# Performance work log

Measured on AMD Instinct MI355X. Metric: run time of the kernel, lower is better.

## Reference

```python
import jax, jax.numpy as jnp
import numpy as np

W = H = 64
CONFIGS = [(1, 3), (2, 3), (3, 3)]  # (dilation, kernel_size)
OUT_PER_CFG = 32
IN_CH = 32


def build_mask():
    # One (W+1, H+1) mask per config, broadcast over (out, in) channels.
    masks = []
    for d, k in CONFIGS:
        m = np.zeros((W + 1, H + 1), dtype=np.float32)
        k1 = (k - 1) * (d - 1) + k  # effective dilated kernel extent
        s1 = (W - k1) // 2 + 1
        e1 = (W + k1) // 2 + 1
        s2 = (H - k1) // 2 + 1
        e2 = (H + k1) // 2 + 1
        m[s1:e1:d, s2:e2:d] = 1.0
        masks.append(np.broadcast_to(m, (OUT_PER_CFG, 1, W + 1, H + 1)))
    return jnp.asarray(np.concatenate(masks, axis=0))  # (96, 1, 65, 65)


def setup_inputs() -> dict:
    key = jax.random.key(0)
    k1, k2 = jax.random.split(key)
    x = jax.random.normal(k1, (16, IN_CH, W, H), dtype=jnp.float32)
    # small init so tanh does not saturate
    weight = jax.random.normal(k2, (OUT_PER_CFG * len(CONFIGS), IN_CH, W + 1, H + 1), dtype=jnp.float32) * 0.01
    mask = build_mask()
    gamma = jnp.ones((OUT_PER_CFG * len(CONFIGS),), dtype=jnp.float32)
    beta = jnp.zeros((OUT_PER_CFG * len(CONFIGS),), dtype=jnp.float32)
    return {"x": x, "weight": weight, "mask": mask, "gamma": gamma, "beta": beta}


def reference(x, weight, mask, gamma, beta):
    # circular pad: last dim by H//2 each side, dim -2 by W//2 each side
    xp = jnp.pad(x, ((0, 0), (0, 0), (W // 2, W // 2), (H // 2, H // 2)), mode="wrap")
    y = jax.lax.conv_general_dilated(
        xp, weight * mask,
        window_strides=(1, 1), padding="VALID",
        dimension_numbers=("NCHW", "OIHW", "NCHW"),
    )  # (B, 96, 64, 64)
    # BatchNorm2d in training mode: batch statistics over (N, H, W), eps=1e-5
    mean = jnp.mean(y, axis=(0, 2, 3))
    var = jnp.var(y, axis=(0, 2, 3))
    yn = (y - mean[None, :, None, None]) * jax.lax.rsqrt(var + 1e-5)[None, :, None, None]
    yn = yn * gamma[None, :, None, None] + beta[None, :, None, None]
    return jnp.tanh(yn)
```

## Files before the change

### kernel.cpp

```cpp
#include <hip/hip_runtime.h>
#include <math.h>

#define BATCH 16
#define CIN 32
#define COUT 96
#define WH 64
#define IMG (WH*WH)
#define NPIX (BATCH*IMG)
#define YELEMS (BATCH*COUT*IMG)
#define NPART 256
#define PWELEMS (3*9*32*32)
#define XTELEMS (BATCH*IMG*CIN)

typedef __attribute__((ext_vector_type(8))) short short8;
typedef __attribute__((ext_vector_type(4))) float floatx4;

__device__ __forceinline__ unsigned short f2bf(float f) {
    union { float f; unsigned u; } v; v.f = f;
    unsigned r = v.u + 0x7FFFu + ((v.u >> 16) & 1u);
    return (unsigned short)(r >> 16);
}

#define GLDS(src, dst) __builtin_amdgcn_global_load_lds( \
    (const __attribute__((address_space(1))) void*)(src), \
    (__attribute__((address_space(3))) void*)(dst), 16, 0, 0)

__global__ __launch_bounds__(256) void packw_kernel(
    const float* __restrict__ w, unsigned short* __restrict__ pw)
{
    int e = blockIdx.x * 256 + threadIdx.x;
    if (e >= PWELEMS) return;
    int cfg = e / (9 * 1024);
    int rem = e % (9 * 1024);
    int tap = rem >> 10;
    int oc  = (rem >> 5) & 31;
    int c   = rem & 31;
    int d   = cfg + 1;
    int du  = tap / 3, dv = tap % 3;
    size_t idx = (((size_t)(cfg * 32 + oc) * CIN + c) * 65 + (32 + (du - 1) * d)) * 65
                 + (32 + (dv - 1) * d);
    pw[e] = f2bf(w[idx]);
}

__global__ __launch_bounds__(256) void xt_kernel(
    const float* __restrict__ x, unsigned short* __restrict__ xT)
{
    int t   = blockIdx.x * 256 + threadIdx.x;
    int b   = t >> 12;
    int pix = t & 4095;
    const float* xb = x + (size_t)b * CIN * IMG + pix;
    unsigned packed[16];
#pragma unroll
    for (int c2 = 0; c2 < 16; c2++) {
        unsigned short lo = f2bf(xb[(size_t)(2 * c2) * IMG]);
        unsigned short hi = f2bf(xb[(size_t)(2 * c2 + 1) * IMG]);
        packed[c2] = (unsigned)lo | ((unsigned)hi << 16);
    }
    uint4* dst = (uint4*)(xT + (size_t)t * 32);
#pragma unroll
    for (int k = 0; k < 4; k++)
        dst[k] = make_uint4(packed[4 * k], packed[4 * k + 1],
                            packed[4 * k + 2], packed[4 * k + 3]);
}

__global__ __launch_bounds__(256, 3) void conv_mfma_kernel(
    const unsigned short* __restrict__ xT, const unsigned short* __restrict__ pw,
    float* __restrict__ y, float* __restrict__ psum, float* __restrict__ psq)
{
    int bid  = blockIdx.x;
    int rowg = bid & 15;
    int rest = bid >> 4;
    int cfg  = rest % 3;
    int b    = rest / 3;
    int d    = cfg + 1;
    int i0   = rowg * 4;

    int t    = threadIdx.x;
    int wv   = t >> 6;
    int lane = t & 63;
    int l15  = lane & 15;
    int quad = lane >> 4;

    __shared__ __align__(16) unsigned short tile[10 * 64 * 32];
    __shared__ float red_s[4][32];
    __shared__ float red_q[4][32];

    const unsigned short* xTb = xT + (size_t)b * IMG * 32;
#pragma unroll
    for (int rr = 0; rr < 10; rr++) {
        int gi = (i0 - 3 + rr) & 63;
        GLDS(xTb + (size_t)gi * 64 * 32 + t * 8, &tile[rr * 2048 + t * 8]);
    }

    const unsigned short* pwc = pw + (size_t)cfg * 9 * 32 * 32;
    short8 af[2][9];
#pragma unroll
    for (int h = 0; h < 2; h++)
#pragma unroll
        for (int tap = 0; tap < 9; tap++)
            af[h][tap] = *(const short8*)(pwc + ((tap * 32 + h * 16 + l15) * 32 + quad * 8));

    __syncthreads();

    float ss[2][4], qq[2][4];
#pragma unroll
    for (int h = 0; h < 2; h++)
#pragma unroll
        for (int r = 0; r < 4; r++) { ss[h][r] = 0.f; qq[h][r] = 0.f; }

    int row = i0 + wv;
    size_t ybase = ((size_t)b * COUT + cfg * 32) * IMG + (size_t)row * WH;

#pragma unroll 1
    for (int cg = 0; cg < 4; cg++) {
        floatx4 acc0 = {0.f, 0.f, 0.f, 0.f};
        floatx4 acc1 = {0.f, 0.f, 0.f, 0.f};
#pragma unroll
        for (int du = 0; du < 3; du++) {
            int rowloc = wv + 3 + (du - 1) * d;
            const unsigned short* rbase = &tile[rowloc * 2048 + quad * 8];
#pragma unroll
            for (int dv = 0; dv < 3; dv++) {
                int col = (cg * 16 + l15 + (dv - 1) * d) & 63;
                short8 bf = *(const short8*)(rbase + col * 32);
                acc0 = __builtin_amdgcn_mfma_f32_16x16x32_bf16(af[0][du * 3 + dv], bf, acc0, 0, 0, 0);
                acc1 = __builtin_amdgcn_mfma_f32_16x16x32_bf16(af[1][du * 3 + dv], bf, acc1, 0, 0, 0);
            }
        }
        int colg = cg * 16 + l15;
#pragma unroll
        for (int r = 0; r < 4; r++) {
            float v0 = acc0[r], v1 = acc1[r];
            int m0 = quad * 4 + r;
            y[ybase + (size_t)m0 * IMG + colg]        = v0;
            y[ybase + (size_t)(16 + m0) * IMG + colg] = v1;
            ss[0][r] += v0; qq[0][r] = fmaf(v0, v0, qq[0][r]);
            ss[1][r] += v1; qq[1][r] = fmaf(v1, v1, qq[1][r]);
        }
    }

#pragma unroll
    for (int h = 0; h < 2; h++)
#pragma unroll
        for (int r = 0; r < 4; r++) {
            float s = ss[h][r], q = qq[h][r];
            for (int m = 1; m < 16; m <<= 1) {
                s += __shfl_xor(s, m, 64);
                q += __shfl_xor(q, m, 64);
            }
            if (l15 == 0) {
                red_s[wv][h * 16 + quad * 4 + r] = s;
                red_q[wv][h * 16 + quad * 4 + r] = q;
            }
        }
    __syncthreads();
    if (t < 32) {
        float S = red_s[0][t] + red_s[1][t] + red_s[2][t] + red_s[3][t];
        psum[(size_t)(cfg * 32 + t) * NPART + b * 16 + rowg] = S;
    } else if (t < 64) {
        int o = t - 32;
        float Q = red_q[0][o] + red_q[1][o] + red_q[2][o] + red_q[3][o];
        psq[(size_t)(cfg * 32 + o) * NPART + b * 16 + rowg] = Q;
    }
}

__device__ __forceinline__ float fast_tanh(float xv) {
    float e = __expf(2.0f * xv);
    return fmaf(-2.0f, __builtin_amdgcn_rcpf(e + 1.0f), 1.0f);
}

__global__ __launch_bounds__(256) void bn_tanh_kernel(
    const float* __restrict__ ybuf, const float* __restrict__ psum,
    const float* __restrict__ psq, const float* __restrict__ gamma,
    const float* __restrict__ beta, float* __restrict__ out)
{
    __shared__ float part[8];
    __shared__ float sc[2];
    int t  = threadIdx.x;
    int ch = blockIdx.x % COUT;

    float s = psum[(size_t)ch * NPART + t];
    float q = psq[(size_t)ch * NPART + t];
    for (int m = 1; m < 64; m <<= 1) {
        s += __shfl_xor(s, m, 64);
        q += __shfl_xor(q, m, 64);
    }
    if ((t & 63) == 0) { part[t >> 6] = s; part[4 + (t >> 6)] = q; }
    __syncthreads();
    if (t == 0) {
        const float inv_n = 1.0f / (float)NPIX;
        float S = part[0] + part[1] + part[2] + part[3];
        float Q = part[4] + part[5] + part[6] + part[7];
        float mean = S * inv_n;
        float var  = Q * inv_n - mean * mean;
        float a    = gamma[ch] * rsqrtf(var + 1e-5f);
        sc[0] = a;
        sc[1] = beta[ch] - mean * a;
    }
    __syncthreads();

    float a = sc[0], bsh = sc[1];
    size_t base4 = (size_t)blockIdx.x * 1024;
#pragma unroll
    for (int k = 0; k < 4; k++) {
        size_t e4 = base4 + k * 256 + t;
        float4 v = ((const float4*)ybuf)[e4];
        float4 r;
        r.x = fast_tanh(fmaf(v.x, a, bsh));
        r.y = fast_tanh(fmaf(v.y, a, bsh));
        r.z = fast_tanh(fmaf(v.z, a, bsh));
        r.w = fast_tanh(fmaf(v.w, a, bsh));
        ((float4*)out)[e4] = r;
    }
}

extern "C" void kernel_launch(void* const* d_in, const int* in_sizes, int n_in,
                              void* d_out, int out_size, void* d_ws, size_t ws_size,
                              hipStream_t stream) {
    const float* x     = (const float*)d_in[0];
    const float* w     = (const float*)d_in[1];
    const float* gamma = (const float*)d_in[3];
    const float* beta  = (const float*)d_in[4];
    float* out = (float*)d_out;

    float* ws   = (float*)d_ws;
    float* ybuf = ws;
    float* psum = ybuf + YELEMS;
    float* psq  = psum + COUT * NPART;

    unsigned short* xT = (unsigned short*)d_out;
    unsigned short* pw = xT + XTELEMS;

    packw_kernel<<<(PWELEMS + 255) / 256, 256, 0, stream>>>(w, pw);
    xt_kernel<<<NPIX / 256, 256, 0, stream>>>(x, xT);
    conv_mfma_kernel<<<768, 256, 0, stream>>>(xT, pw, ybuf, psum, psq);
    bn_tanh_kernel<<<BATCH * COUT, 256, 0, stream>>>(ybuf, psum, psq, gamma, beta, out);
}
```

Before: 120.8 us.

## Fuse conv, batch-norm and tanh via cooperative grid sync, merge prep kernels

Combines the weight-pack and input-transpose kernels into one launch. Recasts the conv kernel so each block covers 8 rows (two per wave) and keeps all accumulators in registers. A cooperative-launch variant writes partial statistics, does a grid-wide sync, reduces per-channel mean and variance, then applies BN and tanh directly to the register accumulators. This removes the full fp32 intermediate y write and re-read and one kernel launch, at the cost of a grid barrier, higher register pressure and a 384-block grid on 2 blocks per CU. A split fallback path with the old two-kernel scheme remains for when cooperative launch is unavailable.

```diff
diff --git a/kernel.cpp b/kernel.cpp
--- a/kernel.cpp
+++ b/kernel.cpp
@@ -1,5 +1,8 @@
 #include <hip/hip_runtime.h>
+#include <hip/hip_cooperative_groups.h>
 #include <math.h>
+
+namespace cg = cooperative_groups;
 
 #define BATCH 16
 #define CIN 32
@@ -8,7 +11,7 @@
 #define IMG (WH*WH)
 #define NPIX (BATCH*IMG)
 #define YELEMS (BATCH*COUT*IMG)
-#define NPART 256
+#define NPART 128
 #define PWELEMS (3*9*32*32)
 #define XTELEMS (BATCH*IMG*CIN)
 
@@ -25,148 +28,248 @@
     (const __attribute__((address_space(1))) void*)(src), \
     (__attribute__((address_space(3))) void*)(dst), 16, 0, 0)
 
-__global__ __launch_bounds__(256) void packw_kernel(
-    const float* __restrict__ w, unsigned short* __restrict__ pw)
-{
-    int e = blockIdx.x * 256 + threadIdx.x;
-    if (e >= PWELEMS) return;
-    int cfg = e / (9 * 1024);
-    int rem = e % (9 * 1024);
-    int tap = rem >> 10;
-    int oc  = (rem >> 5) & 31;
-    int c   = rem & 31;
-    int d   = cfg + 1;
-    int du  = tap / 3, dv = tap % 3;
-    size_t idx = (((size_t)(cfg * 32 + oc) * CIN + c) * 65 + (32 + (du - 1) * d)) * 65
-                 + (32 + (dv - 1) * d);
-    pw[e] = f2bf(w[idx]);
-}
-
-__global__ __launch_bounds__(256) void xt_kernel(
-    const float* __restrict__ x, unsigned short* __restrict__ xT)
-{
-    int t   = blockIdx.x * 256 + threadIdx.x;
-    int b   = t >> 12;
-    int pix = t & 4095;
-    const float* xb = x + (size_t)b * CIN * IMG + pix;
-    unsigned packed[16];
-#pragma unroll
-    for (int c2 = 0; c2 < 16; c2++) {
-        unsigned short lo = f2bf(xb[(size_t)(2 * c2) * IMG]);
-        unsigned short hi = f2bf(xb[(size_t)(2 * c2 + 1) * IMG]);
-        packed[c2] = (unsigned)lo | ((unsigned)hi << 16);
-    }
-    uint4* dst = (uint4*)(xT + (size_t)t * 32);
-#pragma unroll
-    for (int k = 0; k < 4; k++)
-        dst[k] = make_uint4(packed[4 * k], packed[4 * k + 1],
-                            packed[4 * k + 2], packed[4 * k + 3]);
-}
-
-__global__ __launch_bounds__(256, 3) void conv_mfma_kernel(
-    const unsigned short* __restrict__ xT, const unsigned short* __restrict__ pw,
-    float* __restrict__ y, float* __restrict__ psum, float* __restrict__ psq)
-{
-    int bid  = blockIdx.x;
-    int rowg = bid & 15;
-    int rest = bid >> 4;
-    int cfg  = rest % 3;
-    int b    = rest / 3;
-    int d    = cfg + 1;
-    int i0   = rowg * 4;
-
-    int t    = threadIdx.x;
-    int wv   = t >> 6;
-    int lane = t & 63;
-    int l15  = lane & 15;
-    int quad = lane >> 4;
-
-    __shared__ __align__(16) unsigned short tile[10 * 64 * 32];
-    __shared__ float red_s[4][32];
-    __shared__ float red_q[4][32];
-
-    const unsigned short* xTb = xT + (size_t)b * IMG * 32;
-#pragma unroll
-    for (int rr = 0; rr < 10; rr++) {
-        int gi = (i0 - 3 + rr) & 63;
-        GLDS(xTb + (size_t)gi * 64 * 32 + t * 8, &tile[rr * 2048 + t * 8]);
-    }
-
-    const unsigned short* pwc = pw + (size_t)cfg * 9 * 32 * 32;
+__device__ __forceinline__ float fast_tanh(float xv) {
+    float e = __expf(2.0f * xv);
+    return fmaf(-2.0f, __builtin_amdgcn_rcpf(e + 1.0f), 1.0f);
+}
+
+__global__ __launch_bounds__(256) void prep_kernel(
+    const float* __restrict__ x, const float* __restrict__ w,
+    unsigned short* __restrict__ xT, unsigned short* __restrict__ pw)
+{
+    int blk = blockIdx.x;
+    if (blk < 256) {
+        int t   = blk * 256 + threadIdx.x;
+        int b   = t >> 12;
+        int pix = t & 4095;
+        const float* xb = x + (size_t)b * CIN * IMG + pix;
+        unsigned packed[16];
+#pragma unroll
+        for (int c2 = 0; c2 < 16; c2++) {
+            unsigned short lo = f2bf(xb[(size_t)(2 * c2) * IMG]);
+            unsigned short hi = f2bf(xb[(size_t)(2 * c2 + 1) * IMG]);
+            packed[c2] = (unsigned)lo | ((unsigned)hi << 16);
+        }
+        uint4* dst = (uint4*)(xT + (size_t)t * 32);
+#pragma unroll
+        for (int k = 0; k < 4; k++)
+            dst[k] = make_uint4(packed[4 * k], packed[4 * k + 1],
+                                packed[4 * k + 2], packed[4 * k + 3]);
+    } else {
+        int e = (blk - 256) * 256 + threadIdx.x;
+        if (e >= PWELEMS) return;
+        int cfg = e / (9 * 1024);
+        int rem = e % (9 * 1024);
+        int tap = rem >> 10;
+        int oc  = (rem >> 5) & 31;
+        int c   = rem & 31;
+        int d   = cfg + 1;
+        int du  = tap / 3, dv = tap % 3;
+        size_t idx = (((size_t)(cfg * 32 + oc) * CIN + c) * 65 + (32 + (du - 1) * d)) * 65
+                     + (32 + (dv - 1) * d);
+        pw[e] = f2bf(w[idx]);
+    }
+}
+
+struct ConvCtx {
+    int cfg, b, i0, d;
+    int t, wv, lane, l15, quad;
+};
+
+__device__ __forceinline__ void conv_compute(
+    const ConvCtx& C, const unsigned short* __restrict__ xT,
+    const unsigned short* __restrict__ pw, unsigned short* tile,
+    float (*red_s)[32], float (*red_q)[32],
+    float* __restrict__ psum, float* __restrict__ psq,
+    floatx4 acc[2][4][2])
+{
+    const unsigned short* xTb = xT + (size_t)C.b * IMG * 32;
+#pragma unroll
+    for (int rr = 0; rr < 14; rr++) {
+        int gi = (C.i0 - 3 + rr) & 63;
+        GLDS(xTb + (size_t)gi * 2048 + C.t * 8, &tile[rr * 2048 + C.t * 8]);
+    }
+
+    const unsigned short* pwc = pw + (size_t)C.cfg * 9 * 32 * 32;
     short8 af[2][9];
 #pragma unroll
     for (int h = 0; h < 2; h++)
 #pragma unroll
         for (int tap = 0; tap < 9; tap++)
-            af[h][tap] = *(const short8*)(pwc + ((tap * 32 + h * 16 + l15) * 32 + quad * 8));
-
-    __syncthreads();
-
-    float ss[2][4], qq[2][4];
-#pragma unroll
-    for (int h = 0; h < 2; h++)
-#pragma unroll
-        for (int r = 0; r < 4; r++) { ss[h][r] = 0.f; qq[h][r] = 0.f; }
-
-    int row = i0 + wv;
-    size_t ybase = ((size_t)b * COUT + cfg * 32) * IMG + (size_t)row * WH;
+            af[h][tap] = *(const short8*)(pwc + ((tap * 32 + h * 16 + C.l15) * 32 + C.quad * 8));
+
+    __syncthreads();
 
 #pragma unroll 1
     for (int cg = 0; cg < 4; cg++) {
-        floatx4 acc0 = {0.f, 0.f, 0.f, 0.f};
-        floatx4 acc1 = {0.f, 0.f, 0.f, 0.f};
-#pragma unroll
-        for (int du = 0; du < 3; du++) {
-            int rowloc = wv + 3 + (du - 1) * d;
-            const unsigned short* rbase = &tile[rowloc * 2048 + quad * 8];
-#pragma unroll
-            for (int dv = 0; dv < 3; dv++) {
-                int col = (cg * 16 + l15 + (dv - 1) * d) & 63;
-                short8 bf = *(const short8*)(rbase + col * 32);
-                acc0 = __builtin_amdgcn_mfma_f32_16x16x32_bf16(af[0][du * 3 + dv], bf, acc0, 0, 0, 0);
-                acc1 = __builtin_amdgcn_mfma_f32_16x16x32_bf16(af[1][du * 3 + dv], bf, acc1, 0, 0, 0);
+#pragma unroll
+        for (int r = 0; r < 2; r++) {
+            floatx4 a0 = {0.f, 0.f, 0.f, 0.f};
+            floatx4 a1 = {0.f, 0.f, 0.f, 0.f};
+#pragma unroll
+            for (int du = 0; du < 3; du++) {
+                int rowloc = 2 * C.wv + r + 3 + (du - 1) * C.d;
+                const unsigned short* rbase = &tile[rowloc * 2048 + C.quad * 8];
+#pragma unroll
+                for (int dv = 0; dv < 3; dv++) {
+                    int col = (cg * 16 + C.l15 + (dv - 1) * C.d) & 63;
+                    short8 bf = *(const short8*)(rbase + col * 32);
+                    a0 = __builtin_amdgcn_mfma_f32_16x16x32_bf16(af[0][du * 3 + dv], bf, a0, 0, 0, 0);
+                    a1 = __builtin_amdgcn_mfma_f32_16x16x32_bf16(af[1][du * 3 + dv], bf, a1, 0, 0, 0);
+                }
             }
-        }
-        int colg = cg * 16 + l15;
-#pragma unroll
-        for (int r = 0; r < 4; r++) {
-            float v0 = acc0[r], v1 = acc1[r];
-            int m0 = quad * 4 + r;
-            y[ybase + (size_t)m0 * IMG + colg]        = v0;
-            y[ybase + (size_t)(16 + m0) * IMG + colg] = v1;
-            ss[0][r] += v0; qq[0][r] = fmaf(v0, v0, qq[0][r]);
-            ss[1][r] += v1; qq[1][r] = fmaf(v1, v1, qq[1][r]);
-        }
-    }
-
+            acc[r][cg][0] = a0;
+            acc[r][cg][1] = a1;
+        }
+    }
+
+    float ss[2][4], qq[2][4];
 #pragma unroll
     for (int h = 0; h < 2; h++)
 #pragma unroll
-        for (int r = 0; r < 4; r++) {
-            float s = ss[h][r], q = qq[h][r];
+        for (int reg = 0; reg < 4; reg++) { ss[h][reg] = 0.f; qq[h][reg] = 0.f; }
+#pragma unroll
+    for (int r = 0; r < 2; r++)
+#pragma unroll
+        for (int cg = 0; cg < 4; cg++)
+#pragma unroll
+            for (int h = 0; h < 2; h++)
+#pragma unroll
+                for (int reg = 0; reg < 4; reg++) {
+                    float v = acc[r][cg][h][reg];
+                    ss[h][reg] += v;
+                    qq[h][reg] = fmaf(v, v, qq[h][reg]);
+                }
+#pragma unroll
+    for (int h = 0; h < 2; h++)
+#pragma unroll
+        for (int reg = 0; reg < 4; reg++) {
+            float s = ss[h][reg], q = qq[h][reg];
             for (int m = 1; m < 16; m <<= 1) {
                 s += __shfl_xor(s, m, 64);
                 q += __shfl_xor(q, m, 64);
             }
-            if (l15 == 0) {
-                red_s[wv][h * 16 + quad * 4 + r] = s;
-                red_q[wv][h * 16 + quad * 4 + r] = q;
+            if (C.l15 == 0) {
+                red_s[C.wv][h * 16 + C.quad * 4 + reg] = s;
+                red_q[C.wv][h * 16 + C.quad * 4 + reg] = q;
             }
         }
     __syncthreads();
+    int t = C.t;
+    int rowg = C.i0 >> 3;
     if (t < 32) {
         float S = red_s[0][t] + red_s[1][t] + red_s[2][t] + red_s[3][t];
-        psum[(size_t)(cfg * 32 + t) * NPART + b * 16 + rowg] = S;
+        psum[(size_t)(C.cfg * 32 + t) * NPART + C.b * 8 + rowg] = S;
     } else if (t < 64) {
         int o = t - 32;
         float Q = red_q[0][o] + red_q[1][o] + red_q[2][o] + red_q[3][o];
-        psq[(size_t)(cfg * 32 + o) * NPART + b * 16 + rowg] = Q;
-    }
-}
-
-__device__ __forceinline__ float fast_tanh(float xv) {
-    float e = __expf(2.0f * xv);
-    return fmaf(-2.0f, __builtin_amdgcn_rcpf(e + 1.0f), 1.0f);
+        psq[(size_t)(C.cfg * 32 + o) * NPART + C.b * 8 + rowg] = Q;
+    }
+}
+
+__device__ __forceinline__ ConvCtx make_ctx(int bid, int t) {
+    ConvCtx C;
+    int rowg = bid & 7;
+    int rest = bid >> 3;
+    C.cfg = rest % 3;
+    C.b   = rest / 3;
+    C.d   = C.cfg + 1;
+    C.i0  = rowg * 8;
+    C.t   = t;
+    C.wv  = t >> 6;
+    C.lane = t & 63;
+    C.l15 = C.lane & 15;
+    C.quad = C.lane >> 4;
+    return C;
+}
+
+__global__ __launch_bounds__(256, 2) void conv_fused_kernel(
+    const unsigned short* __restrict__ xT, const unsigned short* __restrict__ pw,
+    float* __restrict__ psum, float* __restrict__ psq,
+    const float* __restrict__ gamma, const float* __restrict__ beta,
+    float* __restrict__ out)
+{
+    __shared__ __align__(16) unsigned short tile[14 * 2048];
+    __shared__ float red_s[4][32];
+    __shared__ float red_q[4][32];
+    __shared__ float sc_a[32], sc_b[32];
+
+    ConvCtx C = make_ctx(blockIdx.x, threadIdx.x);
+    floatx4 acc[2][4][2];
+    conv_compute(C, xT, pw, tile, red_s, red_q, psum, psq, acc);
+
+    cg::this_grid().sync();
+
+    {
+        int chl   = C.t >> 3;
+        int slice = C.t & 7;
+        const float* ps = psum + (size_t)(C.cfg * 32 + chl) * NPART + slice * 16;
+        const float* pq = psq  + (size_t)(C.cfg * 32 + chl) * NPART + slice * 16;
+        float s = 0.f, q = 0.f;
+#pragma unroll
+        for (int k = 0; k < 16; k++) { s += ps[k]; q += pq[k]; }
+        for (int m = 1; m < 8; m <<= 1) {
+            s += __shfl_xor(s, m, 8);
+            q += __shfl_xor(q, m, 8);
+        }
+        if (slice == 0) {
+            const float inv_n = 1.0f / (float)NPIX;
+            float mean = s * inv_n;
+            float var  = q * inv_n - mean * mean;
+            float a    = gamma[C.cfg * 32 + chl] * rsqrtf(var + 1e-5f);
+            sc_a[chl] = a;
+            sc_b[chl] = beta[C.cfg * 32 + chl] - mean * a;
+        }
+    }
+    __syncthreads();
+
+#pragma unroll
+    for (int r = 0; r < 2; r++) {
+        int row = C.i0 + 2 * C.wv + r;
+        size_t obase = ((size_t)C.b * COUT + C.cfg * 32) * IMG + (size_t)row * WH;
+#pragma unroll
+        for (int cg = 0; cg < 4; cg++) {
+            int colg = cg * 16 + C.l15;
+#pragma unroll
+            for (int h = 0; h < 2; h++)
+#pragma unroll
+                for (int reg = 0; reg < 4; reg++) {
+                    int oc = h * 16 + C.quad * 4 + reg;
+                    float v = fmaf(acc[r][cg][h][reg], sc_a[oc], sc_b[oc]);
+                    out[obase + (size_t)oc * IMG + colg] = fast_tanh(v);
+                }
+        }
+    }
+}
+
+__global__ __launch_bounds__(256, 2) void conv_split_kernel(
+    const unsigned short* __restrict__ xT, const unsigned short* __restrict__ pw,
+    float* __restrict__ y, float* __restrict__ psum, float* __restrict__ psq)
+{
+    __shared__ __align__(16) unsigned short tile[14 * 2048];
+    __shared__ float red_s[4][32];
+    __shared__ float red_q[4][32];
+
+    ConvCtx C = make_ctx(blockIdx.x, threadIdx.x);
+    floatx4 acc[2][4][2];
+    conv_compute(C, xT, pw, tile, red_s, red_q, psum, psq, acc);
+
+#pragma unroll
+    for (int r = 0; r < 2; r++) {
+        int row = C.i0 + 2 * C.wv + r;
+        size_t ybase = ((size_t)C.b * COUT + C.cfg * 32) * IMG + (size_t)row * WH;
+#pragma unroll
+        for (int cg = 0; cg < 4; cg++) {
+            int colg = cg * 16 + C.l15;
+#pragma unroll
+            for (int h = 0; h < 2; h++)
+#pragma unroll
+                for (int reg = 0; reg < 4; reg++) {
+                    int oc = h * 16 + C.quad * 4 + reg;
+                    y[ybase + (size_t)oc * IMG + colg] = acc[r][cg][h][reg];
+                }
+        }
+    }
 }
 
 __global__ __launch_bounds__(256) void bn_tanh_kernel(
@@ -174,23 +277,22 @@
     const float* __restrict__ psq, const float* __restrict__ gamma,
     const float* __restrict__ beta, float* __restrict__ out)
 {
-    __shared__ float part[8];
+    __shared__ float part[4];
     __shared__ float sc[2];
     int t  = threadIdx.x;
     int ch = blockIdx.x % COUT;
 
-    float s = psum[(size_t)ch * NPART + t];
-    float q = psq[(size_t)ch * NPART + t];
+    float s = 0.f, q = 0.f;
+    if (t < NPART) { s = psum[(size_t)ch * NPART + t]; q = psq[(size_t)ch * NPART + t]; }
     for (int m = 1; m < 64; m <<= 1) {
         s += __shfl_xor(s, m, 64);
         q += __shfl_xor(q, m, 64);
     }
-    if ((t & 63) == 0) { part[t >> 6] = s; part[4 + (t >> 6)] = q; }
+    if (t < NPART && (t & 63) == 0) { part[t >> 6] = s; part[2 + (t >> 6)] = q; }
     __syncthreads();
     if (t == 0) {
         const float inv_n = 1.0f / (float)NPIX;
-        float S = part[0] + part[1] + part[2] + part[3];
-        float Q = part[4] + part[5] + part[6] + part[7];
+        float S = part[0] + part[1], Q = part[2] + part[3];
         float mean = S * inv_n;
         float var  = Q * inv_n - mean * mean;
         float a    = gamma[ch] * rsqrtf(var + 1e-5f);
@@ -224,15 +326,28 @@
     float* out = (float*)d_out;
 
     float* ws   = (float*)d_ws;
-    float* ybuf = ws;
-    float* psum = ybuf + YELEMS;
+    float* psum = ws;
     float* psq  = psum + COUT * NPART;
+    float* ybuf = psq + COUT * NPART;
 
     unsigned short* xT = (unsigned short*)d_out;
     unsigned short* pw = xT + XTELEMS;
 
-    packw_kernel<<<(PWELEMS + 255) / 256, 256, 0, stream>>>(w, pw);
-    xt_kernel<<<NPIX / 256, 256, 0, stream>>>(x, xT);
-    conv_mfma_kernel<<<768, 256, 0, stream>>>(xT, pw, ybuf, psum, psq);
+    prep_kernel<<<256 + (PWELEMS + 255) / 256, 256, 0, stream>>>(x, w, xT, pw);
+
+    int blocksPerCU = 0;
+    hipError_t qe = hipOccupancyMaxActiveBlocksPerMultiprocessor(
+        &blocksPerCU, (const void*)conv_fused_kernel, 256, 0);
+    bool coop_ok = (qe == hipSuccess) && ((long)blocksPerCU * 256 >= 384);
+
+    if (coop_ok) {
+        void* args[] = {(void*)&xT, (void*)&pw, (void*)&psum, (void*)&psq,
+                        (void*)&gamma, (void*)&beta, (void*)&out};
+        hipError_t le = hipLaunchCooperativeKernel((const void*)conv_fused_kernel,
+                                                   dim3(384), dim3(256), args, 0, stream);
+        if (le == hipSuccess) return;
+    }
+
+    conv_split_kernel<<<384, 256, 0, stream>>>(xT, pw, ybuf, psum, psq);
     bn_tanh_kernel<<<BATCH * COUT, 256, 0, stream>>>(ybuf, psum, psq, gamma, beta, out);
 }
```

Result: slower. 191.2 us (+58.3%).

## Recompute convolution in BN pass instead of storing intermediate y

Applied to the files above, without the earlier changes.

Removes the intermediate fp32 conv output buffer. The first conv pass now only accumulates per-channel sum and sum-of-squares, and a second conv pass recomputes the convolution and applies BN and tanh directly before writing the output. The two prep kernels are also merged into one launch. This trades one extra cheap MFMA conv pass for not writing and re-reading about 25 MB of y.

```diff
diff --git a/kernel.cpp b/kernel.cpp
--- a/kernel.cpp
+++ b/kernel.cpp
@@ -7,7 +7,6 @@
 #define WH 64
 #define IMG (WH*WH)
 #define NPIX (BATCH*IMG)
-#define YELEMS (BATCH*COUT*IMG)
 #define NPART 256
 #define PWELEMS (3*9*32*32)
 #define XTELEMS (BATCH*IMG*CIN)
@@ -25,47 +24,52 @@
     (const __attribute__((address_space(1))) void*)(src), \
     (__attribute__((address_space(3))) void*)(dst), 16, 0, 0)
 
-__global__ __launch_bounds__(256) void packw_kernel(
-    const float* __restrict__ w, unsigned short* __restrict__ pw)
+__device__ __forceinline__ float fast_tanh(float xv) {
+    float e = __expf(2.0f * xv);
+    return fmaf(-2.0f, __builtin_amdgcn_rcpf(e + 1.0f), 1.0f);
+}
+
+__global__ __launch_bounds__(256) void prep_kernel(
+    const float* __restrict__ x, const float* __restrict__ w,
+    unsigned short* __restrict__ xT, unsigned short* __restrict__ pw)
 {
-    int e = blockIdx.x * 256 + threadIdx.x;
-    if (e >= PWELEMS) return;
-    int cfg = e / (9 * 1024);
-    int rem = e % (9 * 1024);
-    int tap = rem >> 10;
-    int oc  = (rem >> 5) & 31;
-    int c   = rem & 31;
-    int d   = cfg + 1;
-    int du  = tap / 3, dv = tap % 3;
-    size_t idx = (((size_t)(cfg * 32 + oc) * CIN + c) * 65 + (32 + (du - 1) * d)) * 65
-                 + (32 + (dv - 1) * d);
-    pw[e] = f2bf(w[idx]);
-}
-
-__global__ __launch_bounds__(256) void xt_kernel(
-    const float* __restrict__ x, unsigned short* __restrict__ xT)
-{
-    int t   = blockIdx.x * 256 + threadIdx.x;
-    int b   = t >> 12;
-    int pix = t & 4095;
-    const float* xb = x + (size_t)b * CIN * IMG + pix;
-    unsigned packed[16];
-#pragma unroll
-    for (int c2 = 0; c2 < 16; c2++) {
-        unsigned short lo = f2bf(xb[(size_t)(2 * c2) * IMG]);
-        unsigned short hi = f2bf(xb[(size_t)(2 * c2 + 1) * IMG]);
-        packed[c2] = (unsigned)lo | ((unsigned)hi << 16);
-    }
-    uint4* dst = (uint4*)(xT + (size_t)t * 32);
-#pragma unroll
-    for (int k = 0; k < 4; k++)
-        dst[k] = make_uint4(packed[4 * k], packed[4 * k + 1],
-                            packed[4 * k + 2], packed[4 * k + 3]);
-}
-
-__global__ __launch_bounds__(256, 3) void conv_mfma_kernel(
+    int blk = blockIdx.x;
+    if (blk < 256) {
+        int t   = blk * 256 + threadIdx.x;
+        int b   = t >> 12;
+        int pix = t & 4095;
+        const float* xb = x + (size_t)b * CIN * IMG + pix;
+        unsigned packed[16];
+#pragma unroll
+        for (int c2 = 0; c2 < 16; c2++) {
+            unsigned short lo = f2bf(xb[(size_t)(2 * c2) * IMG]);
+            unsigned short hi = f2bf(xb[(size_t)(2 * c2 + 1) * IMG]);
+            packed[c2] = (unsigned)lo | ((unsigned)hi << 16);
+        }
+        uint4* dst = (uint4*)(xT + (size_t)t * 32);
+#pragma unroll
+        for (int k = 0; k < 4; k++)
+            dst[k] = make_uint4(packed[4 * k], packed[4 * k + 1],
+                                packed[4 * k + 2], packed[4 * k + 3]);
+    } else {
+        int e = (blk - 256) * 256 + threadIdx.x;
+        if (e >= PWELEMS) return;
+        int cfg = e / (9 * 1024);
+        int rem = e % (9 * 1024);
+        int tap = rem >> 10;
+        int oc  = (rem >> 5) & 31;
+        int c   = rem & 31;
+        int d   = cfg + 1;
+        int du  = tap / 3, dv = tap % 3;
+        size_t idx = (((size_t)(cfg * 32 + oc) * CIN + c) * 65 + (32 + (du - 1) * d)) * 65
+                     + (32 + (dv - 1) * d);
+        pw[e] = f2bf(w[idx]);
+    }
+}
+
+__global__ __launch_bounds__(256, 3) void conv_stats_kernel(
     const unsigned short* __restrict__ xT, const unsigned short* __restrict__ pw,
-    float* __restrict__ y, float* __restrict__ psum, float* __restrict__ psq)
+    float* __restrict__ psum, float* __restrict__ psq)
 {
     int bid  = blockIdx.x;
     int rowg = bid & 15;
@@ -81,7 +85,7 @@
     int l15  = lane & 15;
     int quad = lane >> 4;
 
-    __shared__ __align__(16) unsigned short tile[10 * 64 * 32];
+    __shared__ __align__(16) unsigned short tile[10 * 2048];
     __shared__ float red_s[4][32];
     __shared__ float red_q[4][32];
 
@@ -89,7 +93,7 @@
 #pragma unroll
     for (int rr = 0; rr < 10; rr++) {
         int gi = (i0 - 3 + rr) & 63;
-        GLDS(xTb + (size_t)gi * 64 * 32 + t * 8, &tile[rr * 2048 + t * 8]);
+        GLDS(xTb + (size_t)gi * 2048 + t * 8, &tile[rr * 2048 + t * 8]);
     }
 
     const unsigned short* pwc = pw + (size_t)cfg * 9 * 32 * 32;
@@ -108,13 +112,10 @@
 #pragma unroll
         for (int r = 0; r < 4; r++) { ss[h][r] = 0.f; qq[h][r] = 0.f; }
 
-    int row = i0 + wv;
-    size_t ybase = ((size_t)b * COUT + cfg * 32) * IMG + (size_t)row * WH;
-
 #pragma unroll 1
     for (int cg = 0; cg < 4; cg++) {
-        floatx4 acc0 = {0.f, 0.f, 0.f, 0.f};
-        floatx4 acc1 = {0.f, 0.f, 0.f, 0.f};
+        floatx4 a0 = {0.f, 0.f, 0.f, 0.f};
+        floatx4 a1 = {0.f, 0.f, 0.f, 0.f};
 #pragma unroll
         for (int du = 0; du < 3; du++) {
             int rowloc = wv + 3 + (du - 1) * d;
@@ -123,17 +124,13 @@
             for (int dv = 0; dv < 3; dv++) {
                 int col = (cg * 16 + l15 + (dv - 1) * d) & 63;
                 short8 bf = *(const short8*)(rbase + col * 32);
-                acc0 = __builtin_amdgcn_mfma_f32_16x16x32_bf16(af[0][du * 3 + dv], bf, acc0, 0, 0, 0);
-                acc1 = __builtin_amdgcn_mfma_f32_16x16x32_bf16(af[1][du * 3 + dv], bf, acc1, 0, 0, 0);
-            }
-        }
-        int colg = cg * 16 + l15;
+                a0 = __builtin_amdgcn_mfma_f32_16x16x32_bf16(af[0][du * 3 + dv], bf, a0, 0, 0, 0);
+                a1 = __builtin_amdgcn_mfma_f32_16x16x32_bf16(af[1][du * 3 + dv], bf, a1, 0, 0, 0);
+            }
+        }
 #pragma unroll
         for (int r = 0; r < 4; r++) {
-            float v0 = acc0[r], v1 = acc1[r];
-            int m0 = quad * 4 + r;
-            y[ybase + (size_t)m0 * IMG + colg]        = v0;
-            y[ybase + (size_t)(16 + m0) * IMG + colg] = v1;
+            float v0 = a0[r], v1 = a1[r];
             ss[0][r] += v0; qq[0][r] = fmaf(v0, v0, qq[0][r]);
             ss[1][r] += v1; qq[1][r] = fmaf(v1, v1, qq[1][r]);
         }
@@ -164,53 +161,96 @@
     }
 }
 
-__device__ __forceinline__ float fast_tanh(float xv) {
-    float e = __expf(2.0f * xv);
-    return fmaf(-2.0f, __builtin_amdgcn_rcpf(e + 1.0f), 1.0f);
-}
-
-__global__ __launch_bounds__(256) void bn_tanh_kernel(
-    const float* __restrict__ ybuf, const float* __restrict__ psum,
-    const float* __restrict__ psq, const float* __restrict__ gamma,
-    const float* __restrict__ beta, float* __restrict__ out)
+__global__ __launch_bounds__(256, 3) void conv_bn_kernel(
+    const unsigned short* __restrict__ xT, const unsigned short* __restrict__ pw,
+    const float* __restrict__ psum, const float* __restrict__ psq,
+    const float* __restrict__ gamma, const float* __restrict__ beta,
+    float* __restrict__ out)
 {
-    __shared__ float part[8];
-    __shared__ float sc[2];
-    int t  = threadIdx.x;
-    int ch = blockIdx.x % COUT;
-
-    float s = psum[(size_t)ch * NPART + t];
-    float q = psq[(size_t)ch * NPART + t];
-    for (int m = 1; m < 64; m <<= 1) {
-        s += __shfl_xor(s, m, 64);
-        q += __shfl_xor(q, m, 64);
-    }
-    if ((t & 63) == 0) { part[t >> 6] = s; part[4 + (t >> 6)] = q; }
+    int bid  = blockIdx.x;
+    int rowg = bid & 15;
+    int rest = bid >> 4;
+    int cfg  = rest % 3;
+    int b    = rest / 3;
+    int d    = cfg + 1;
+    int i0   = rowg * 4;
+
+    int t    = threadIdx.x;
+    int wv   = t >> 6;
+    int lane = t & 63;
+    int l15  = lane & 15;
+    int quad = lane >> 4;
+
+    __shared__ __align__(16) unsigned short tile[10 * 2048];
+    __shared__ float sc_a[32], sc_b[32];
+
+    const unsigned short* xTb = xT + (size_t)b * IMG * 32;
+#pragma unroll
+    for (int rr = 0; rr < 10; rr++) {
+        int gi = (i0 - 3 + rr) & 63;
+        GLDS(xTb + (size_t)gi * 2048 + t * 8, &tile[rr * 2048 + t * 8]);
+    }
+
+    {
+        int chl   = t >> 3;
+        int slice = t & 7;
+        const float* ps = psum + (size_t)(cfg * 32 + chl) * NPART + slice * 32;
+        const float* pq = psq  + (size_t)(cfg * 32 + chl) * NPART + slice * 32;
+        float s = 0.f, q = 0.f;
+#pragma unroll
+        for (int k = 0; k < 32; k++) { s += ps[k]; q += pq[k]; }
+        for (int m = 1; m < 8; m <<= 1) {
+            s += __shfl_xor(s, m, 8);
+            q += __shfl_xor(q, m, 8);
+        }
+        if (slice == 0) {
+            const float inv_n = 1.0f / (float)NPIX;
+            float mean = s * inv_n;
+            float var  = q * inv_n - mean * mean;
+            float a    = gamma[cfg * 32 + chl] * rsqrtf(var + 1e-5f);
+            sc_a[chl] = a;
+            sc_b[chl] = beta[cfg * 32 + chl] - mean * a;
+        }
+    }
+
+    const unsigned short* pwc = pw + (size_t)cfg * 9 * 32 * 32;
+    short8 af[2][9];
+#pragma unroll
+    for (int h = 0; h < 2; h++)
+#pragma unroll
+        for (int tap = 0; tap < 9; tap++)
+            af[h][tap] = *(const short8*)(pwc + ((tap * 32 + h * 16 + l15) * 32 + quad * 8));
+
     __syncthreads();
-    if (t == 0) {
-        const float inv_n = 1.0f / (float)NPIX;
-        float S = part[0] + part[1] + part[2] + part[3];
-        float Q = part[4] + part[5] + part[6] + part[7];
-        float mean = S * inv_n;
-        float var  = Q * inv_n - mean * mean;
-        float a    = gamma[ch] * rsqrtf(var + 1e-5f);
-        sc[0] = a;
-        sc[1] = beta[ch] - mean * a;
-    }
-    __syncthreads();
-
-    float a = sc[0], bsh = sc[1];
-    size_t base4 = (size_t)blockIdx.x * 1024;
-#pragma unroll
-    for (int k = 0; k < 4; k++) {
-        size_t e4 = base4 + k * 256 + t;
-        float4 v = ((const float4*)ybuf)[e4];
-        float4 r;
-        r.x = fast_tanh(fmaf(v.x, a, bsh));
-        r.y = fast_tanh(fmaf(v.y, a, bsh));
-        r.z = fast_tanh(fmaf(v.z, a, bsh));
-        r.w = fast_tanh(fmaf(v.w, a, bsh));
-        ((float4*)out)[e4] = r;
+
+    int row = i0 + wv;
+    size_t obase = ((size_t)b * COUT + cfg * 32) * IMG + (size_t)row * WH;
+
+#pragma unroll 1
+    for (int cg = 0; cg < 4; cg++) {
+        floatx4 a0 = {0.f, 0.f, 0.f, 0.f};
+        floatx4 a1 = {0.f, 0.f, 0.f, 0.f};
+#pragma unroll
+        for (int du = 0; du < 3; du++) {
+            int rowloc = wv + 3 + (du - 1) * d;
+            const unsigned short* rbase = &tile[rowloc * 2048 + quad * 8];
+#pragma unroll
+            for (int dv = 0; dv < 3; dv++) {
+                int col = (cg * 16 + l15 + (dv - 1) * d) & 63;
+                short8 bf = *(const short8*)(rbase + col * 32);
+                a0 = __builtin_amdgcn_mfma_f32_16x16x32_bf16(af[0][du * 3 + dv], bf, a0, 0, 0, 0);
+                a1 = __builtin_amdgcn_mfma_f32_16x16x32_bf16(af[1][du * 3 + dv], bf, a1, 0, 0, 0);
+            }
+        }
+        int colg = cg * 16 + l15;
+#pragma unroll
+        for (int r = 0; r < 4; r++) {
+            int m0 = quad * 4 + r;
+            float v0 = fmaf(a0[r], sc_a[m0],      sc_b[m0]);
+            float v1 = fmaf(a1[r], sc_a[16 + m0], sc_b[16 + m0]);
+            out[obase + (size_t)m0 * IMG + colg]        = fast_tanh(v0);
+            out[obase + (size_t)(16 + m0) * IMG + colg] = fast_tanh(v1);
+        }
     }
 }
 
@@ -223,16 +263,12 @@
     const float* beta  = (const float*)d_in[4];
     float* out = (float*)d_out;
 
-    float* ws   = (float*)d_ws;
-    float* ybuf = ws;
-    float* psum = ybuf + YELEMS;
+    unsigned short* xT = (unsigned short*)d_ws;
+    unsigned short* pw = xT + XTELEMS;
+    float* psum = (float*)(pw + PWELEMS + 32);
     float* psq  = psum + COUT * NPART;
 
-    unsigned short* xT = (unsigned short*)d_out;
-    unsigned short* pw = xT + XTELEMS;
-
-    packw_kernel<<<(PWELEMS + 255) / 256, 256, 0, stream>>>(w, pw);
-    xt_kernel<<<NPIX / 256, 256, 0, stream>>>(x, xT);
-    conv_mfma_kernel<<<768, 256, 0, stream>>>(xT, pw, ybuf, psum, psq);
-    bn_tanh_kernel<<<BATCH * COUT, 256, 0, stream>>>(ybuf, psum, psq, gamma, beta, out);
-}
+    prep_kernel<<<256 + (PWELEMS + 255) / 256, 256, 0, stream>>>(x, w, xT, pw);
+    conv_stats_kernel<<<768, 256, 0, stream>>>(xT, pw, psum, psq);
+    conv_bn_kernel<<<768, 256, 0, stream>>>(xT, pw, psum, psq, gamma, beta, out);
+}
```

Result: no change. 123.2 us (+2.0%).
